# Performance work log

Hardware: AMD Instinct MI355X
Metric: run time of the kernel (lower is better)

## Reference

```python
import jax, jax.numpy as jnp
import numpy as np

B, S, DIM = 2, 8192, 1024
NH, NKV, HD = 16, 4, 64
GROUPS = NH // NKV
CHUNK = 128
THETA = 10000.0


def _slopes(h):
    # ALiBi-style per-head decay slopes (h is a power of two)
    return jnp.asarray([2.0 ** (-8.0 / h * (i + 1)) for i in range(h)], dtype=jnp.float32)


def _rope_tables(s, d):
    inv = 1.0 / (THETA ** (np.arange(0, d, 2, dtype=np.float64) / d))
    freqs = np.outer(np.arange(s, dtype=np.float64), inv)  # [s, d/2]
    emb = np.concatenate([freqs, freqs], axis=-1)  # [s, d]
    return jnp.asarray(np.cos(emb), jnp.float32), jnp.asarray(np.sin(emb), jnp.float32)


def _apply_rope(x, cos, sin):
    # x: [b, h, s, d]; cos/sin: [s, d]
    x1, x2 = jnp.split(x, 2, axis=-1)
    rot = jnp.concatenate([-x2, x1], axis=-1)
    return x * cos + rot * sin


def _lightning_attn(q, k, v, slopes, chunk):
    # out[t] = sum_{i<=t} exp(-slope*(t-i)) * (q_t . k_i) * v_i, chunked O(n) recurrence
    b, h, s, d = q.shape
    nc = s // chunk
    t = jnp.arange(chunk, dtype=jnp.float32)
    sl = slopes[:, None, None]  # [h,1,1]
    mask = jnp.where(t[:, None] >= t[None, :],
                     jnp.exp(-sl * (t[:, None] - t[None, :])), 0.0)  # [h,C,C]
    q_dec = jnp.exp(-slopes[:, None] * (t + 1.0))[..., None]          # [h,C,1]
    k_dec = jnp.exp(-slopes[:, None] * (chunk - 1.0 - t))[..., None]  # [h,C,1]
    blk_dec = jnp.exp(-slopes * chunk)[None, :, None, None]           # [1,h,1,1]

    def to_chunks(x):
        return x.reshape(b, h, nc, chunk, d).transpose(2, 0, 1, 3, 4)  # [nc,b,h,C,d]

    qc, kc, vc = to_chunks(q), to_chunks(k), to_chunks(v)

    def step(kv, inp):
        qi, ki, vi = inp  # [b,h,C,d]
        scores = jnp.einsum('bhtd,bhsd->bhts', qi, ki) * mask
        o = jnp.einsum('bhts,bhsd->bhtd', scores, vi) \
            + jnp.einsum('bhtd,bhde->bhte', qi * q_dec, kv)
        kv = blk_dec * kv + jnp.einsum('bhtd,bhte->bhde', ki * k_dec, vi)
        return kv, o

    kv0 = jnp.zeros((b, h, d, d), q.dtype)
    _, outs = jax.lax.scan(step, kv0, (qc, kc, vc))  # outs: [nc,b,h,C,d]
    return outs.transpose(1, 2, 0, 3, 4).reshape(b, h, s, d)


def setup_inputs() -> dict:
    key = jax.random.key(0)
    k0, k1, k2, k3, k4 = jax.random.split(key, 5)
    x = jax.random.normal(k0, (B, S, DIM), jnp.float32)
    Wq = jax.random.normal(k1, (NH * HD, DIM), jnp.float32) * 0.02
    Wk = jax.random.normal(k2, (NKV * HD, DIM), jnp.float32) * 0.02
    Wv = jax.random.normal(k3, (NKV * HD, DIM), jnp.float32) * 0.02
    Wo = jax.random.normal(k4, (DIM, NH * HD), jnp.float32) * 0.02
    return {"x": x, "Wq": Wq, "Wk": Wk, "Wv": Wv, "Wo": Wo}


def reference(x, Wq, Wk, Wv, Wo):
    b, s, _ = x.shape
    q = (x @ Wq.T).reshape(b, s, NH, HD).transpose(0, 2, 1, 3)
    k = (x @ Wk.T).reshape(b, s, NKV, HD).transpose(0, 2, 1, 3)
    v = (x @ Wv.T).reshape(b, s, NKV, HD).transpose(0, 2, 1, 3)
    cos, sin = _rope_tables(s, HD)
    q = _apply_rope(q, cos, sin)
    k = _apply_rope(k, cos, sin)
    # GQA expand: head index = kv_head*groups + g  <=>  repeat along head axis
    k = jnp.repeat(k, GROUPS, axis=1)
    v = jnp.repeat(v, GROUPS, axis=1)
    out = _lightning_attn(q, k, v, _slopes(NH), CHUNK)  # [b,NH,s,HD]
    out = out.transpose(0, 2, 1, 3).reshape(b, s, NH * HD)
    return out @ Wo.T
```

## Files before the change

### kernel.cpp

```cpp
#include <hip/hip_runtime.h>
#include <hip/hip_bf16.h>

#define B_ 2
#define S_ 8192
#define DIM_ 1024
#define NH_ 16
#define NKV_ 4
#define HD_ 64
#define NC_ 64

typedef __bf16 bf16x8 __attribute__((ext_vector_type(8)));
typedef float f32x4 __attribute__((ext_vector_type(4)));
using bf16 = __hip_bfloat16;

#define ASYNC16(gp, lp) __builtin_amdgcn_global_load_lds( \
    (__attribute__((address_space(1))) void*)(void*)(gp), \
    (__attribute__((address_space(3))) void*)(void*)(lp), 16, 0, 0)

__global__ __launch_bounds__(256) void f2b4_kernel(const float* __restrict__ in, bf16* __restrict__ out) {
    size_t i = ((size_t)blockIdx.x * 256 + threadIdx.x) * 4;
    const float4 f = *(const float4*)(in + i);
    bf16 t[4];
    t[0] = __float2bfloat16(f.x); t[1] = __float2bfloat16(f.y);
    t[2] = __float2bfloat16(f.z); t[3] = __float2bfloat16(f.w);
    *(uint2*)(out + i) = *(const uint2*)t;
}

__global__ __launch_bounds__(256) void wconv_kernel(const float* __restrict__ Wq, const float* __restrict__ Wk,
                                                    const float* __restrict__ Wv, const float* __restrict__ Wo,
                                                    bf16* __restrict__ wqkv, bf16* __restrict__ wo) {
    size_t e = ((size_t)blockIdx.x * 256 + threadIdx.x) * 4;
    const float* src;
    bf16* dst;
    if (e < 1048576)      { src = Wq + e;           dst = wqkv + e; }
    else if (e < 1310720) { src = Wk + (e - 1048576); dst = wqkv + e; }
    else if (e < 1572864) { src = Wv + (e - 1310720); dst = wqkv + e; }
    else                  { src = Wo + (e - 1572864); dst = wo + (e - 1572864); }
    const float4 f = *(const float4*)src;
    bf16 t[4];
    t[0] = __float2bfloat16(f.x); t[1] = __float2bfloat16(f.y);
    t[2] = __float2bfloat16(f.z); t[3] = __float2bfloat16(f.w);
    *(uint2*)dst = *(const uint2*)t;
}

__global__ __launch_bounds__(256) void rope_tab_kernel(float* __restrict__ cosd, float* __restrict__ sind) {
    int idx = blockIdx.x * 256 + threadIdx.x;
    int s = idx >> 5, i = idx & 31;
    double inv = exp((double)i * (-9.210340371976184 / 32.0));
    double rev = ((double)s * inv) * 0.15915494309189535;
    double frac = rev - floor(rev);
    float a = (float)frac * 6.2831853071795865f;
    cosd[idx] = __cosf(a);
    sind[idx] = __sinf(a);
}

template <typename OT>
__global__ __launch_bounds__(256) void gemm_bt_kernel(const bf16* __restrict__ A, const bf16* __restrict__ Bm,
                                                      OT* __restrict__ C, int M, int N, int K, int rope_ncols,
                                                      const float* __restrict__ cosd,
                                                      const float* __restrict__ sind) {
    __shared__ bf16 As[128 * 64];
    __shared__ bf16 Bs[128 * 64];
    const int tid = threadIdx.x;
    const int bm = blockIdx.x * 128, bn = blockIdx.y * 128;
    const int wave = tid >> 6, lane = tid & 63;
    const int wm = (wave >> 1) * 64, wn = (wave & 1) * 64;
    const int lr = lane & 15, quad = lane >> 4;
    const int srow = wave * 32;
    const int lrow = lane >> 3;
    const int lchunk = ((lane & 7) ^ lrow) * 8;
    const bf16* Ag = A + (size_t)(bm + srow + lrow) * K + lchunk;
    const bf16* Bg = Bm + (size_t)(bn + srow + lrow) * K + lchunk;
    f32x4 acc[4][4] = {};
    for (int k0 = 0; k0 < K; k0 += 64) {
#pragma unroll
        for (int p = 0; p < 4; ++p) {
            ASYNC16(Ag + (size_t)(p * 8) * K + k0, &As[(srow + p * 8) * 64]);
            ASYNC16(Bg + (size_t)(p * 8) * K + k0, &Bs[(srow + p * 8) * 64]);
        }
        __syncthreads();
#pragma unroll
        for (int kk = 0; kk < 64; kk += 32) {
            const int sw = (((kk >> 3) + quad) ^ (lr & 7)) << 3;
            bf16x8 af[4], bfr[4];
#pragma unroll
            for (int i = 0; i < 4; ++i) af[i] = *(const bf16x8*)(&As[(wm + i * 16 + lr) * 64 + sw]);
#pragma unroll
            for (int i = 0; i < 4; ++i) bfr[i] = *(const bf16x8*)(&Bs[(wn + i * 16 + lr) * 64 + sw]);
#pragma unroll
            for (int mi = 0; mi < 4; ++mi)
#pragma unroll
                for (int ni = 0; ni < 4; ++ni)
                    acc[mi][ni] = __builtin_amdgcn_mfma_f32_16x16x32_bf16(af[mi], bfr[ni], acc[mi][ni], 0, 0, 0);
        }
        __syncthreads();
    }
    if (bn + wn < rope_ncols) {
#pragma unroll
        for (int mi = 0; mi < 4; ++mi)
#pragma unroll
            for (int r = 0; r < 4; ++r) {
                int row = bm + wm + mi * 16 + quad * 4 + r;
                int s = row & (S_ - 1);
#pragma unroll
                for (int ni = 0; ni < 2; ++ni) {
                    int i = ni * 16 + lr;
                    float cs = cosd[(s << 5) + i];
                    float sn = sind[(s << 5) + i];
                    float x1 = acc[mi][ni][r], x2 = acc[mi][ni + 2][r];
                    acc[mi][ni][r] = x1 * cs - x2 * sn;
                    acc[mi][ni + 2][r] = x2 * cs + x1 * sn;
                }
            }
    }
#pragma unroll
    for (int mi = 0; mi < 4; ++mi)
#pragma unroll
        for (int ni = 0; ni < 4; ++ni)
#pragma unroll
            for (int r = 0; r < 4; ++r) {
                int row = bm + wm + mi * 16 + quad * 4 + r;
                int col = bn + wn + ni * 16 + lr;
                float v = acc[mi][ni][r];
                if constexpr (__is_same(OT, float)) C[(size_t)row * N + col] = v;
                else C[(size_t)row * N + col] = __float2bfloat16(v);
            }
}

__global__ __launch_bounds__(256) void chunk_kv_kernel(const bf16* __restrict__ qkv, bf16* __restrict__ Cout) {
    const int j = blockIdx.x, h = blockIdx.y, b = blockIdx.z;
    const int g = h >> 2;
    const float slope = exp2f(-0.5f * (float)(h + 1));
    __shared__ bf16 kdT[64][136];
    __shared__ bf16 vT[64][136];
    const int tid = threadIdx.x;
#pragma unroll
    for (int p = 0; p < 4; ++p) {
        int flat = p * 256 + tid;
        int t = flat >> 3, d0 = (flat & 7) * 8;
        const size_t row = (size_t)(b * S_ + j * 128 + t);
        uint4 kw = *(const uint4*)(qkv + row * 1536 + 1024 + g * 64 + d0);
        uint4 vw = *(const uint4*)(qkv + row * 1536 + 1280 + g * 64 + d0);
        float kdec = __expf(-slope * (float)(127 - t));
        const bf16* kp = (const bf16*)&kw;
        const bf16* vp = (const bf16*)&vw;
#pragma unroll
        for (int i = 0; i < 8; ++i) {
            kdT[d0 + i][t] = __float2bfloat16(__bfloat162float(kp[i]) * kdec);
            vT[d0 + i][t] = vp[i];
        }
    }
    __syncthreads();
    const int wave = tid >> 6, lane = tid & 63, lr = lane & 15, quad = lane >> 4;
    const int e0 = wave * 16;
    f32x4 acc[4] = {};
#pragma unroll
    for (int ks = 0; ks < 128; ks += 32) {
        bf16x8 a = *(const bf16x8*)(&vT[e0 + lr][ks + quad * 8]);
#pragma unroll
        for (int ni = 0; ni < 4; ++ni) {
            bf16x8 bb = *(const bf16x8*)(&kdT[ni * 16 + lr][ks + quad * 8]);
            acc[ni] = __builtin_amdgcn_mfma_f32_16x16x32_bf16(a, bb, acc[ni], 0, 0, 0);
        }
    }
    bf16* out = Cout + ((size_t)((b * NH_ + h) * NC_ + j)) * 4096;
#pragma unroll
    for (int ni = 0; ni < 4; ++ni)
#pragma unroll
        for (int r = 0; r < 4; ++r)
            out[(e0 + quad * 4 + r) * 64 + ni * 16 + lr] = __float2bfloat16(acc[ni][r]);
}

__global__ __launch_bounds__(256) void scan_kv_kernel(const bf16* __restrict__ Cin, bf16* __restrict__ st) {
    const int bh = blockIdx.x >> 4;
    const int f = ((blockIdx.x & 15) << 8) + threadIdx.x;
    const int h = bh & (NH_ - 1);
    const float slope = exp2f(-0.5f * (float)(h + 1));
    const float bdec = __expf(-slope * 128.0f);
    const bf16* Cb = Cin + (size_t)bh * NC_ * 4096 + f;
    bf16* sb = st + (size_t)bh * NC_ * 4096 + f;
    float carry = 0.f;
#pragma unroll 8
    for (int c = 0; c < NC_; ++c) {
        sb[(size_t)c * 4096] = __float2bfloat16(carry);
        carry = bdec * carry + __bfloat162float(Cb[(size_t)c * 4096]);
    }
}

__global__ __launch_bounds__(256) void attn_chunk_kernel(const bf16* __restrict__ qkv, const bf16* __restrict__ kvst,
                                                         bf16* __restrict__ outb) {
    const int c = blockIdx.x, h = blockIdx.y, b = blockIdx.z;
    const int g = h >> 2;
    const float slope = exp2f(-0.5f * (float)(h + 1));
    __shared__ bf16 qs[128][72];
    __shared__ bf16 ub[128 * 72];
    __shared__ bf16 Ps[128][136];
    const int tid = threadIdx.x;
    const int wave = tid >> 6, lane = tid & 63, lr = lane & 15, quad = lane >> 4;
#pragma unroll
    for (int p = 0; p < 4; ++p) {
        int flat = p * 256 + tid;
        int t = flat >> 3, d0 = (flat & 7) * 8;
        size_t row = (size_t)(b * S_ + c * 128 + t);
        *(uint4*)(&qs[t][d0]) = *(const uint4*)(qkv + row * 1536 + h * 64 + d0);
        *(uint4*)(&ub[t * 72 + d0]) = *(const uint4*)(qkv + row * 1536 + 1024 + g * 64 + d0);
    }
    __syncthreads();
    const int m0 = wave * 32;
    f32x4 sacc[2][8] = {};
#pragma unroll
    for (int kk = 0; kk < 64; kk += 32) {
        bf16x8 af0 = *(const bf16x8*)(&qs[m0 + lr][kk + quad * 8]);
        bf16x8 af1 = *(const bf16x8*)(&qs[m0 + 16 + lr][kk + quad * 8]);
#pragma unroll
        for (int ni = 0; ni < 8; ++ni) {
            bf16x8 bfr = *(const bf16x8*)(&ub[(ni * 16 + lr) * 72 + kk + quad * 8]);
            sacc[0][ni] = __builtin_amdgcn_mfma_f32_16x16x32_bf16(af0, bfr, sacc[0][ni], 0, 0, 0);
            sacc[1][ni] = __builtin_amdgcn_mfma_f32_16x16x32_bf16(af1, bfr, sacc[1][ni], 0, 0, 0);
        }
    }
    __syncthreads();
#pragma unroll
    for (int mi = 0; mi < 2; ++mi)
#pragma unroll
        for (int ni = 0; ni < 8; ++ni)
#pragma unroll
            for (int r = 0; r < 4; ++r) {
                int t = m0 + mi * 16 + quad * 4 + r;
                int tp = ni * 16 + lr;
                int del = t - tp;
                float val = (del >= 0) ? sacc[mi][ni][r] * __expf(-slope * (float)del) : 0.f;
                Ps[t][tp] = __float2bfloat16(val);
            }
#pragma unroll
    for (int p = 0; p < 4; ++p) {
        int flat = p * 256 + tid;
        int t = flat >> 3, d0 = (flat & 7) * 8;
        size_t row = (size_t)(b * S_ + c * 128 + t);
        uint4 vw = *(const uint4*)(qkv + row * 1536 + 1280 + g * 64 + d0);
        const bf16* vp = (const bf16*)&vw;
#pragma unroll
        for (int i = 0; i < 8; ++i) ub[(d0 + i) * 136 + t] = vp[i];
    }
    __syncthreads();
    f32x4 oacc[2][4] = {};
#pragma unroll
    for (int ks2 = 0; ks2 < 128; ks2 += 32) {
        bf16x8 af0 = *(const bf16x8*)(&Ps[m0 + lr][ks2 + quad * 8]);
        bf16x8 af1 = *(const bf16x8*)(&Ps[m0 + 16 + lr][ks2 + quad * 8]);
#pragma unroll
        for (int ni = 0; ni < 4; ++ni) {
            bf16x8 bfv = *(const bf16x8*)(&ub[(ni * 16 + lr) * 136 + ks2 + quad * 8]);
            oacc[0][ni] = __builtin_amdgcn_mfma_f32_16x16x32_bf16(af0, bfv, oacc[0][ni], 0, 0, 0);
            oacc[1][ni] = __builtin_amdgcn_mfma_f32_16x16x32_bf16(af1, bfv, oacc[1][ni], 0, 0, 0);
        }
    }
    const bf16* kvb = kvst + ((size_t)((b * NH_ + h) * NC_ + c)) * 4096;
#pragma unroll
    for (int kk = 0; kk < 64; kk += 32) {
        bf16x8 af[2];
#pragma unroll
        for (int mi = 0; mi < 2; ++mi) {
            bf16x8 a0 = *(const bf16x8*)(&qs[m0 + mi * 16 + lr][kk + quad * 8]);
            float qd = __expf(-slope * (float)(m0 + mi * 16 + lr + 1));
#pragma unroll
            for (int i = 0; i < 8; ++i) a0[i] = (__bf16)((float)a0[i] * qd);
            af[mi] = a0;
        }
#pragma unroll
        for (int ni = 0; ni < 4; ++ni) {
            bf16x8 bk = *(const bf16x8*)(kvb + (ni * 16 + lr) * 64 + kk + quad * 8);
            oacc[0][ni] = __builtin_amdgcn_mfma_f32_16x16x32_bf16(af[0], bk, oacc[0][ni], 0, 0, 0);
            oacc[1][ni] = __builtin_amdgcn_mfma_f32_16x16x32_bf16(af[1], bk, oacc[1][ni], 0, 0, 0);
        }
    }
#pragma unroll
    for (int mi = 0; mi < 2; ++mi)
#pragma unroll
        for (int ni = 0; ni < 4; ++ni)
#pragma unroll
            for (int r = 0; r < 4; ++r) {
                int t = m0 + mi * 16 + quad * 4 + r;
                int e = ni * 16 + lr;
                size_t row = (size_t)(b * S_ + c * 128 + t);
                outb[row * (NH_ * 64) + h * 64 + e] = __float2bfloat16(oacc[mi][ni][r]);
            }
}

extern "C" void kernel_launch(void* const* d_in, const int* in_sizes, int n_in,
                              void* d_out, int out_size, void* d_ws, size_t ws_size,
                              hipStream_t stream) {
    (void)in_sizes; (void)n_in; (void)out_size; (void)ws_size;
    const float* x  = (const float*)d_in[0];
    const float* Wq = (const float*)d_in[1];
    const float* Wk = (const float*)d_in[2];
    const float* Wv = (const float*)d_in[3];
    const float* Wo = (const float*)d_in[4];
    float* out = (float*)d_out;
    char* ws = (char*)d_ws;
    bf16*  xb    = (bf16*)(ws);
    bf16*  qkvb  = (bf16*)(ws + 33554432);
    bf16*  wqkvb = (bf16*)(ws + 83886080);
    bf16*  wob   = (bf16*)(ws + 87031808);
    float* cosd  = (float*)(ws + 89128960);
    float* sind  = (float*)(ws + 90177536);
    bf16*  Cbuf  = (bf16*)(ws + 91226112);
    bf16*  kvst  = (bf16*)(ws + 108003328);
    bf16*  attn  = xb;

    f2b4_kernel<<<16384, 256, 0, stream>>>(x, xb);
    wconv_kernel<<<2560, 256, 0, stream>>>(Wq, Wk, Wv, Wo, wqkvb, wob);
    rope_tab_kernel<<<(S_ * 32) / 256, 256, 0, stream>>>(cosd, sind);

    gemm_bt_kernel<bf16><<<dim3(128, 12), 256, 0, stream>>>(xb, wqkvb, qkvb, 16384, 1536, 1024, 1280, cosd, sind);

    chunk_kv_kernel<<<dim3(NC_, NH_, B_), 256, 0, stream>>>(qkvb, Cbuf);
    scan_kv_kernel<<<512, 256, 0, stream>>>(Cbuf, kvst);
    attn_chunk_kernel<<<dim3(NC_, NH_, B_), 256, 0, stream>>>(qkvb, kvst, attn);

    gemm_bt_kernel<float><<<dim3(128, 8), 256, 0, stream>>>(attn, wob, out, 16384, 1024, 1024, 0, cosd, sind);
}
```

Measured before the change: 307.9 us.

## Fuse prep kernels, swizzle LDS, alias attention shared memory, add occupancy hints

Merges the three preprocessing kernels (x conversion, weight conversion, RoPE tables) into one launch to cut launch overhead. It XOR-swizzles the transposed LDS tiles in chunk_kv and attn_chunk to reduce bank conflicts, and aliases the attention kernel's shared buffers to shrink LDS footprint. It also moves the inter-chunk state matmul earlier and factors the decay exp into per-row and per-column terms. Adds min-blocks-per-CU launch bounds, which risk register spills.

```diff
diff --git a/kernel.cpp b/kernel.cpp
--- a/kernel.cpp
+++ b/kernel.cpp
@@ -17,48 +17,49 @@
     (__attribute__((address_space(1))) void*)(void*)(gp), \
     (__attribute__((address_space(3))) void*)(void*)(lp), 16, 0, 0)
 
-__global__ __launch_bounds__(256) void f2b4_kernel(const float* __restrict__ in, bf16* __restrict__ out) {
-    size_t i = ((size_t)blockIdx.x * 256 + threadIdx.x) * 4;
-    const float4 f = *(const float4*)(in + i);
-    bf16 t[4];
-    t[0] = __float2bfloat16(f.x); t[1] = __float2bfloat16(f.y);
-    t[2] = __float2bfloat16(f.z); t[3] = __float2bfloat16(f.w);
-    *(uint2*)(out + i) = *(const uint2*)t;
-}
-
-__global__ __launch_bounds__(256) void wconv_kernel(const float* __restrict__ Wq, const float* __restrict__ Wk,
-                                                    const float* __restrict__ Wv, const float* __restrict__ Wo,
-                                                    bf16* __restrict__ wqkv, bf16* __restrict__ wo) {
-    size_t e = ((size_t)blockIdx.x * 256 + threadIdx.x) * 4;
-    const float* src;
-    bf16* dst;
-    if (e < 1048576)      { src = Wq + e;           dst = wqkv + e; }
-    else if (e < 1310720) { src = Wk + (e - 1048576); dst = wqkv + e; }
-    else if (e < 1572864) { src = Wv + (e - 1310720); dst = wqkv + e; }
-    else                  { src = Wo + (e - 1572864); dst = wo + (e - 1572864); }
-    const float4 f = *(const float4*)src;
-    bf16 t[4];
-    t[0] = __float2bfloat16(f.x); t[1] = __float2bfloat16(f.y);
-    t[2] = __float2bfloat16(f.z); t[3] = __float2bfloat16(f.w);
-    *(uint2*)dst = *(const uint2*)t;
-}
-
-__global__ __launch_bounds__(256) void rope_tab_kernel(float* __restrict__ cosd, float* __restrict__ sind) {
-    int idx = blockIdx.x * 256 + threadIdx.x;
-    int s = idx >> 5, i = idx & 31;
-    double inv = exp((double)i * (-9.210340371976184 / 32.0));
-    double rev = ((double)s * inv) * 0.15915494309189535;
-    double frac = rev - floor(rev);
-    float a = (float)frac * 6.2831853071795865f;
-    cosd[idx] = __cosf(a);
-    sind[idx] = __sinf(a);
+__global__ __launch_bounds__(256) void prep_kernel(const float* __restrict__ x, const float* __restrict__ Wq,
+                                                   const float* __restrict__ Wk, const float* __restrict__ Wv,
+                                                   const float* __restrict__ Wo, bf16* __restrict__ xb,
+                                                   bf16* __restrict__ wqkv, bf16* __restrict__ wo,
+                                                   float* __restrict__ cosd, float* __restrict__ sind) {
+    int bid = blockIdx.x;
+    if (bid < 16384) {
+        size_t i = ((size_t)bid * 256 + threadIdx.x) * 4;
+        const float4 f = *(const float4*)(x + i);
+        bf16 t[4];
+        t[0] = __float2bfloat16(f.x); t[1] = __float2bfloat16(f.y);
+        t[2] = __float2bfloat16(f.z); t[3] = __float2bfloat16(f.w);
+        *(uint2*)(xb + i) = *(const uint2*)t;
+    } else if (bid < 18944) {
+        size_t e = ((size_t)(bid - 16384) * 256 + threadIdx.x) * 4;
+        const float* src;
+        bf16* dst;
+        if (e < 1048576)        { src = Wq + e;             dst = wqkv + e; }
+        else if (e < 1310720)   { src = Wk + (e - 1048576); dst = wqkv + e; }
+        else if (e < 1572864)   { src = Wv + (e - 1310720); dst = wqkv + e; }
+        else                    { src = Wo + (e - 1572864); dst = wo + (e - 1572864); }
+        const float4 f = *(const float4*)src;
+        bf16 t[4];
+        t[0] = __float2bfloat16(f.x); t[1] = __float2bfloat16(f.y);
+        t[2] = __float2bfloat16(f.z); t[3] = __float2bfloat16(f.w);
+        *(uint2*)dst = *(const uint2*)t;
+    } else {
+        int idx = (bid - 18944) * 256 + threadIdx.x;
+        int s = idx >> 5, i = idx & 31;
+        double inv = exp((double)i * (-9.210340371976184 / 32.0));
+        double rev = ((double)s * inv) * 0.15915494309189535;
+        double frac = rev - floor(rev);
+        float a = (float)frac * 6.2831853071795865f;
+        cosd[idx] = __cosf(a);
+        sind[idx] = __sinf(a);
+    }
 }
 
 template <typename OT>
-__global__ __launch_bounds__(256) void gemm_bt_kernel(const bf16* __restrict__ A, const bf16* __restrict__ Bm,
-                                                      OT* __restrict__ C, int M, int N, int K, int rope_ncols,
-                                                      const float* __restrict__ cosd,
-                                                      const float* __restrict__ sind) {
+__global__ __launch_bounds__(256, 3) void gemm_bt_kernel(const bf16* __restrict__ A, const bf16* __restrict__ Bm,
+                                                         OT* __restrict__ C, int M, int N, int K, int rope_ncols,
+                                                         const float* __restrict__ cosd,
+                                                         const float* __restrict__ sind) {
     __shared__ bf16 As[128 * 64];
     __shared__ bf16 Bs[128 * 64];
     const int tid = threadIdx.x;
@@ -127,12 +128,13 @@
             }
 }
 
-__global__ __launch_bounds__(256) void chunk_kv_kernel(const bf16* __restrict__ qkv, bf16* __restrict__ Cout) {
+
+__global__ __launch_bounds__(256, 4) void chunk_kv_kernel(const bf16* __restrict__ qkv, bf16* __restrict__ Cout) {
     const int j = blockIdx.x, h = blockIdx.y, b = blockIdx.z;
     const int g = h >> 2;
     const float slope = exp2f(-0.5f * (float)(h + 1));
-    __shared__ bf16 kdT[64][136];
-    __shared__ bf16 vT[64][136];
+    __shared__ bf16 kdT[64 * 136];
+    __shared__ bf16 vT[64 * 136];
     const int tid = threadIdx.x;
 #pragma unroll
     for (int p = 0; p < 4; ++p) {
@@ -146,20 +148,26 @@
         const bf16* vp = (const bf16*)&vw;
 #pragma unroll
         for (int i = 0; i < 8; ++i) {
-            kdT[d0 + i][t] = __float2bfloat16(__bfloat162float(kp[i]) * kdec);
-            vT[d0 + i][t] = vp[i];
+            int e = d0 + i;
+            int sw = (((t >> 3) & ~7) << 3) + ((((t >> 3) ^ (e >> 3)) & 7) << 3) + (t & 7);
+            kdT[e * 136 + sw] = __float2bfloat16(__bfloat162float(kp[i]) * kdec);
+            vT[e * 136 + sw] = vp[i];
         }
     }
     __syncthreads();
     const int wave = tid >> 6, lane = tid & 63, lr = lane & 15, quad = lane >> 4;
-    const int e0 = wave * 16;
+    const int ew = wave * 16;
     f32x4 acc[4] = {};
 #pragma unroll
     for (int ks = 0; ks < 128; ks += 32) {
-        bf16x8 a = *(const bf16x8*)(&vT[e0 + lr][ks + quad * 8]);
+        int qa = (ks >> 3) + quad;
+        int qhi = (qa & ~7) << 3;
+        int ea = ew + lr;
+        bf16x8 a = *(const bf16x8*)(&vT[ea * 136 + qhi + (((qa ^ (ea >> 3)) & 7) << 3)]);
 #pragma unroll
         for (int ni = 0; ni < 4; ++ni) {
-            bf16x8 bb = *(const bf16x8*)(&kdT[ni * 16 + lr][ks + quad * 8]);
+            int eb = ni * 16 + lr;
+            bf16x8 bb = *(const bf16x8*)(&kdT[eb * 136 + qhi + (((qa ^ (eb >> 3)) & 7) << 3)]);
             acc[ni] = __builtin_amdgcn_mfma_f32_16x16x32_bf16(a, bb, acc[ni], 0, 0, 0);
         }
     }
@@ -168,7 +176,7 @@
     for (int ni = 0; ni < 4; ++ni)
 #pragma unroll
         for (int r = 0; r < 4; ++r)
-            out[(e0 + quad * 4 + r) * 64 + ni * 16 + lr] = __float2bfloat16(acc[ni][r]);
+            out[(ew + quad * 4 + r) * 64 + ni * 16 + lr] = __float2bfloat16(acc[ni][r]);
 }
 
 __global__ __launch_bounds__(256) void scan_kv_kernel(const bf16* __restrict__ Cin, bf16* __restrict__ st) {
@@ -187,14 +195,17 @@
     }
 }
 
-__global__ __launch_bounds__(256) void attn_chunk_kernel(const bf16* __restrict__ qkv, const bf16* __restrict__ kvst,
-                                                         bf16* __restrict__ outb) {
+__global__ __launch_bounds__(256, 3) void attn_chunk_kernel(const bf16* __restrict__ qkv,
+                                                            const bf16* __restrict__ kvst,
+                                                            bf16* __restrict__ outb) {
     const int c = blockIdx.x, h = blockIdx.y, b = blockIdx.z;
     const int g = h >> 2;
     const float slope = exp2f(-0.5f * (float)(h + 1));
-    __shared__ bf16 qs[128][72];
-    __shared__ bf16 ub[128 * 72];
-    __shared__ bf16 Ps[128][136];
+    __shared__ bf16 smem[26112];
+    bf16* qs  = smem;
+    bf16* kbs = smem + 9216;
+    bf16* Ps  = smem;
+    bf16* vT  = smem + 17408;
     const int tid = threadIdx.x;
     const int wave = tid >> 6, lane = tid & 63, lr = lane & 15, quad = lane >> 4;
 #pragma unroll
@@ -202,24 +213,52 @@
         int flat = p * 256 + tid;
         int t = flat >> 3, d0 = (flat & 7) * 8;
         size_t row = (size_t)(b * S_ + c * 128 + t);
-        *(uint4*)(&qs[t][d0]) = *(const uint4*)(qkv + row * 1536 + h * 64 + d0);
-        *(uint4*)(&ub[t * 72 + d0]) = *(const uint4*)(qkv + row * 1536 + 1024 + g * 64 + d0);
+        *(uint4*)(&qs[t * 72 + d0]) = *(const uint4*)(qkv + row * 1536 + h * 64 + d0);
+        *(uint4*)(&kbs[t * 72 + d0]) = *(const uint4*)(qkv + row * 1536 + 1024 + g * 64 + d0);
     }
     __syncthreads();
     const int m0 = wave * 32;
     f32x4 sacc[2][8] = {};
 #pragma unroll
     for (int kk = 0; kk < 64; kk += 32) {
-        bf16x8 af0 = *(const bf16x8*)(&qs[m0 + lr][kk + quad * 8]);
-        bf16x8 af1 = *(const bf16x8*)(&qs[m0 + 16 + lr][kk + quad * 8]);
+        bf16x8 af0 = *(const bf16x8*)(&qs[(m0 + lr) * 72 + kk + quad * 8]);
+        bf16x8 af1 = *(const bf16x8*)(&qs[(m0 + 16 + lr) * 72 + kk + quad * 8]);
 #pragma unroll
         for (int ni = 0; ni < 8; ++ni) {
-            bf16x8 bfr = *(const bf16x8*)(&ub[(ni * 16 + lr) * 72 + kk + quad * 8]);
+            bf16x8 bfr = *(const bf16x8*)(&kbs[(ni * 16 + lr) * 72 + kk + quad * 8]);
             sacc[0][ni] = __builtin_amdgcn_mfma_f32_16x16x32_bf16(af0, bfr, sacc[0][ni], 0, 0, 0);
             sacc[1][ni] = __builtin_amdgcn_mfma_f32_16x16x32_bf16(af1, bfr, sacc[1][ni], 0, 0, 0);
         }
     }
+    f32x4 oacc[2][4] = {};
+    const bf16* kvb = kvst + ((size_t)((b * NH_ + h) * NC_ + c)) * 4096;
+    float qd0 = __expf(-slope * (float)(m0 + lr + 1));
+    float qd1 = __expf(-slope * (float)(m0 + 16 + lr + 1));
+#pragma unroll
+    for (int kk = 0; kk < 64; kk += 32) {
+        bf16x8 a0 = *(const bf16x8*)(&qs[(m0 + lr) * 72 + kk + quad * 8]);
+        bf16x8 a1 = *(const bf16x8*)(&qs[(m0 + 16 + lr) * 72 + kk + quad * 8]);
+#pragma unroll
+        for (int i = 0; i < 8; ++i) {
+            a0[i] = (__bf16)((float)a0[i] * qd0);
+            a1[i] = (__bf16)((float)a1[i] * qd1);
+        }
+#pragma unroll
+        for (int ni = 0; ni < 4; ++ni) {
+            bf16x8 bk = *(const bf16x8*)(kvb + (ni * 16 + lr) * 64 + kk + quad * 8);
+            oacc[0][ni] = __builtin_amdgcn_mfma_f32_16x16x32_bf16(a0, bk, oacc[0][ni], 0, 0, 0);
+            oacc[1][ni] = __builtin_amdgcn_mfma_f32_16x16x32_bf16(a1, bk, oacc[1][ni], 0, 0, 0);
+        }
+    }
     __syncthreads();
+    float ftv[2][4], gtv[8];
+#pragma unroll
+    for (int mi = 0; mi < 2; ++mi)
+#pragma unroll
+        for (int r = 0; r < 4; ++r) ftv[mi][r] = __expf(-slope * (float)(mi * 16 + quad * 4 + r));
+#pragma unroll
+    for (int ni = 0; ni < 8; ++ni)
+        gtv[ni] = __expf(-slope * fmaxf((float)(m0 - (ni * 16 + lr)), -31.0f));
 #pragma unroll
     for (int mi = 0; mi < 2; ++mi)
 #pragma unroll
@@ -228,9 +267,9 @@
             for (int r = 0; r < 4; ++r) {
                 int t = m0 + mi * 16 + quad * 4 + r;
                 int tp = ni * 16 + lr;
-                int del = t - tp;
-                float val = (del >= 0) ? sacc[mi][ni][r] * __expf(-slope * (float)del) : 0.f;
-                Ps[t][tp] = __float2bfloat16(val);
+                float val = (t >= tp) ? sacc[mi][ni][r] * ftv[mi][r] * gtv[ni] : 0.f;
+                int sw = (((tp >> 3) & ~7) << 3) + ((((tp >> 3) ^ (t >> 3)) & 7) << 3) + (tp & 7);
+                Ps[t * 136 + sw] = __float2bfloat16(val);
             }
 #pragma unroll
     for (int p = 0; p < 4; ++p) {
@@ -240,38 +279,26 @@
         uint4 vw = *(const uint4*)(qkv + row * 1536 + 1280 + g * 64 + d0);
         const bf16* vp = (const bf16*)&vw;
 #pragma unroll
-        for (int i = 0; i < 8; ++i) ub[(d0 + i) * 136 + t] = vp[i];
+        for (int i = 0; i < 8; ++i) {
+            int e = d0 + i;
+            int sw = (((t >> 3) & ~7) << 3) + ((((t >> 3) ^ (e >> 3)) & 7) << 3) + (t & 7);
+            vT[e * 136 + sw] = vp[i];
+        }
     }
     __syncthreads();
-    f32x4 oacc[2][4] = {};
 #pragma unroll
     for (int ks2 = 0; ks2 < 128; ks2 += 32) {
-        bf16x8 af0 = *(const bf16x8*)(&Ps[m0 + lr][ks2 + quad * 8]);
-        bf16x8 af1 = *(const bf16x8*)(&Ps[m0 + 16 + lr][ks2 + quad * 8]);
+        int qa = (ks2 >> 3) + quad;
+        int qhi = (qa & ~7) << 3;
+        int ra0 = m0 + lr, ra1 = m0 + 16 + lr;
+        bf16x8 af0 = *(const bf16x8*)(&Ps[ra0 * 136 + qhi + (((qa ^ (ra0 >> 3)) & 7) << 3)]);
+        bf16x8 af1 = *(const bf16x8*)(&Ps[ra1 * 136 + qhi + (((qa ^ (ra1 >> 3)) & 7) << 3)]);
 #pragma unroll
         for (int ni = 0; ni < 4; ++ni) {
-            bf16x8 bfv = *(const bf16x8*)(&ub[(ni * 16 + lr) * 136 + ks2 + quad * 8]);
+            int eb = ni * 16 + lr;
+            bf16x8 bfv = *(const bf16x8*)(&vT[eb * 136 + qhi + (((qa ^ (eb >> 3)) & 7) << 3)]);
             oacc[0][ni] = __builtin_amdgcn_mfma_f32_16x16x32_bf16(af0, bfv, oacc[0][ni], 0, 0, 0);
             oacc[1][ni] = __builtin_amdgcn_mfma_f32_16x16x32_bf16(af1, bfv, oacc[1][ni], 0, 0, 0);
-        }
-    }
-    const bf16* kvb = kvst + ((size_t)((b * NH_ + h) * NC_ + c)) * 4096;
-#pragma unroll
-    for (int kk = 0; kk < 64; kk += 32) {
-        bf16x8 af[2];
-#pragma unroll
-        for (int mi = 0; mi < 2; ++mi) {
-            bf16x8 a0 = *(const bf16x8*)(&qs[m0 + mi * 16 + lr][kk + quad * 8]);
-            float qd = __expf(-slope * (float)(m0 + mi * 16 + lr + 1));
-#pragma unroll
-            for (int i = 0; i < 8; ++i) a0[i] = (__bf16)((float)a0[i] * qd);
-            af[mi] = a0;
-        }
-#pragma unroll
-        for (int ni = 0; ni < 4; ++ni) {
-            bf16x8 bk = *(const bf16x8*)(kvb + (ni * 16 + lr) * 64 + kk + quad * 8);
-            oacc[0][ni] = __builtin_amdgcn_mfma_f32_16x16x32_bf16(af[0], bk, oacc[0][ni], 0, 0, 0);
-            oacc[1][ni] = __builtin_amdgcn_mfma_f32_16x16x32_bf16(af[1], bk, oacc[1][ni], 0, 0, 0);
         }
     }
 #pragma unroll
@@ -308,9 +335,7 @@
     bf16*  kvst  = (bf16*)(ws + 108003328);
     bf16*  attn  = xb;
 
-    f2b4_kernel<<<16384, 256, 0, stream>>>(x, xb);
-    wconv_kernel<<<2560, 256, 0, stream>>>(Wq, Wk, Wv, Wo, wqkvb, wob);
-    rope_tab_kernel<<<(S_ * 32) / 256, 256, 0, stream>>>(cosd, sind);
+    prep_kernel<<<19968, 256, 0, stream>>>(x, Wq, Wk, Wv, Wo, xb, wqkvb, wob, cosd, sind);
 
     gemm_bt_kernel<bf16><<<dim3(128, 12), 256, 0, stream>>>(xb, wqkvb, qkvb, 16384, 1536, 1024, 1280, cosd, sind);
 
```

New measurement: 267.4 us. 13.2% less time.
